# Optimization experiments

Hardware: AMD Instinct MI355X
Metric: run time of the kernel (lower is better)

## Reference

```python
import jax, jax.numpy as jnp
import numpy as np

N_HEAD = 16


def setup_inputs() -> dict:
    key = jax.random.key(0)
    ks = jax.random.split(key, 5)
    B, T, C = 4, 2048, 1024
    s = 1.0 / np.sqrt(C)
    x = jax.random.normal(ks[0], (B, T, C), dtype=jnp.float32)
    wq = jax.random.normal(ks[1], (C, C), dtype=jnp.float32) * s
    wk = jax.random.normal(ks[2], (C, C), dtype=jnp.float32) * s
    wv = jax.random.normal(ks[3], (C, C), dtype=jnp.float32) * s
    wo = jax.random.normal(ks[4], (C, C), dtype=jnp.float32) * s
    return {"x": x, "wq": wq, "wk": wk, "wv": wv, "wo": wo}


def _attn(x, wq, wk, wv, wo):
    B, T, C = x.shape
    H = N_HEAD
    D = C // H
    scale = 1.0 / np.sqrt(D)
    # nn.Linear(x) = x @ W.T; weights stored as [out, in]
    q = (x @ wq.T).reshape(B, T, H, D).transpose(0, 2, 1, 3)  # [B,H,T,D]
    k = (x @ wk.T).reshape(B, T, H, D).transpose(0, 2, 1, 3)
    v = (x @ wv.T).reshape(B, T, H, D).transpose(0, 2, 1, 3)
    scores = jnp.einsum("bhtd,bhsd->bhts", q, k) * scale  # [B,H,T,T]
    mask = jnp.triu(jnp.full((T, T), -jnp.inf, dtype=scores.dtype), k=1)
    attn = jax.nn.softmax(scores + mask, axis=-1)
    out = jnp.einsum("bhts,bhsd->bhtd", attn, v)  # [B,H,T,D]
    out = out.transpose(0, 2, 1, 3).reshape(B, T, C)
    return out @ wo.T


def reference(x, wq, wk, wv, wo):
    return _attn(x, wq, wk, wv, wo)
```

## Files before the change

kernel.cpp:

```cpp
#include <hip/hip_runtime.h>

typedef __bf16 bf16x8 __attribute__((ext_vector_type(8)));
typedef float f32x4 __attribute__((ext_vector_type(4)));
typedef unsigned short ushortx8 __attribute__((ext_vector_type(8)));
typedef unsigned short ushortx4 __attribute__((ext_vector_type(4)));

#if __has_builtin(__builtin_amdgcn_exp2f)
#define EXP2F(x) __builtin_amdgcn_exp2f(x)
#else
#define EXP2F(x) exp2f(x)
#endif
#if __has_builtin(__builtin_amdgcn_rcpf)
#define RCPF(x) __builtin_amdgcn_rcpf(x)
#else
#define RCPF(x) (1.0f / (x))
#endif

__device__ __forceinline__ unsigned short f2bf(float f) {
    unsigned int u = __builtin_bit_cast(unsigned int, f);
    u += 0x7fffu + ((u >> 16) & 1u);
    return (unsigned short)(u >> 16);
}

__device__ __forceinline__ bf16x8 ld_frag(const unsigned short* p) {
    return __builtin_bit_cast(bf16x8, *(const ushortx8*)p);
}

__device__ __forceinline__ unsigned int pack_bf2(float lo, float hi) {
#if __has_builtin(__builtin_amdgcn_cvt_pk_bf16_f32)
    typedef __bf16 bf16x2 __attribute__((ext_vector_type(2)));
    bf16x2 v = __builtin_amdgcn_cvt_pk_bf16_f32(lo, hi);
    return __builtin_bit_cast(unsigned int, v);
#else
    unsigned int ulo = __builtin_bit_cast(unsigned int, lo) + 0x8000u;
    unsigned int uhi = __builtin_bit_cast(unsigned int, hi) + 0x8000u;
    return __builtin_amdgcn_perm(uhi, ulo, 0x07060302u);
#endif
}

__device__ __forceinline__ void async_cp16(const unsigned short* g, unsigned short* l) {
    __builtin_amdgcn_global_load_lds(
        (const __attribute__((address_space(1))) unsigned int*)g,
        (__attribute__((address_space(3))) unsigned int*)(unsigned long)(unsigned long long)(uintptr_t)
            reinterpret_cast<uintptr_t>(l),
        16, 0, 0);
}

__global__ void cvt_kernel(const float* __restrict__ src, unsigned short* __restrict__ dst, int n4) {
    int i = blockIdx.x * blockDim.x + threadIdx.x;
    if (i < n4) {
        float4 f = ((const float4*)src)[i];
        ushortx4 u = { f2bf(f.x), f2bf(f.y), f2bf(f.z), f2bf(f.w) };
        ((ushortx4*)dst)[i] = u;
    }
}

__global__ void cvt4_kernel(const float* __restrict__ s0, const float* __restrict__ s1,
                            const float* __restrict__ s2, const float* __restrict__ s3,
                            unsigned short* __restrict__ dst) {
    const float* src = (blockIdx.y == 0) ? s0 : (blockIdx.y == 1) ? s1 : (blockIdx.y == 2) ? s2 : s3;
    unsigned short* d = dst + (size_t)blockIdx.y * (1024 * 1024);
    int i = blockIdx.x * blockDim.x + threadIdx.x;
    float4 f = ((const float4*)src)[i];
    ushortx4 u = { f2bf(f.x), f2bf(f.y), f2bf(f.z), f2bf(f.w) };
    ((ushortx4*)d)[i] = u;
}

__global__ __launch_bounds__(256, 2) void qkv_gemm(
    const unsigned short* __restrict__ xb,
    const unsigned short* __restrict__ wqb,
    const unsigned short* __restrict__ wkb,
    const unsigned short* __restrict__ wvb,
    unsigned short* __restrict__ q_ws,
    unsigned short* __restrict__ k_ws,
    unsigned short* __restrict__ v_ws)
{
    __shared__ __align__(16) unsigned short A_lds[128 * 32];
    __shared__ __align__(16) unsigned short B_lds[128 * 32];

    const int tid = threadIdx.x;
    const int wv = tid >> 6;
    const int lane = tid & 63;
    const int quad = lane >> 4;
    const int l15 = lane & 15;
    const int wm = wv >> 1;
    const int wn = wv & 1;

    const int m0 = blockIdx.x * 128;
    const int mat = blockIdx.y >> 3;
    const int n0 = (blockIdx.y & 7) * 128;
    const unsigned short* wb = (mat == 0) ? wqb : (mat == 1 ? wkb : wvb);

    const int srow = lane >> 2;
    const int scol = ((((lane & 3) - ((lane >> 3) & 3)) & 3) * 8);
    const unsigned short* ag0 = xb + (size_t)(m0 + wv * 32 + srow) * 1024 + scol;
    const unsigned short* ag1 = ag0 + 16 * 1024;
    const unsigned short* bg0 = wb + (size_t)(n0 + wv * 32 + srow) * 1024 + scol;
    const unsigned short* bg1 = bg0 + 16 * 1024;
    unsigned short* la0 = A_lds + (wv * 32) * 32;
    unsigned short* la1 = A_lds + (wv * 32 + 16) * 32;
    unsigned short* lb0 = B_lds + (wv * 32) * 32;
    unsigned short* lb1 = B_lds + (wv * 32 + 16) * 32;

    const int fcol = ((quad + (l15 >> 1)) & 3) * 8;

    f32x4 acc[4][4] = {};

    for (int kt = 0; kt < 1024; kt += 32) {
        __syncthreads();
        async_cp16(ag0 + kt, la0);
        async_cp16(ag1 + kt, la1);
        async_cp16(bg0 + kt, lb0);
        async_cp16(bg1 + kt, lb1);
        __builtin_amdgcn_s_waitcnt(0x0F70);
        __syncthreads();

        bf16x8 af[4], bf[4];
#pragma unroll
        for (int i = 0; i < 4; ++i)
            af[i] = ld_frag(A_lds + (wm * 64 + i * 16 + l15) * 32 + fcol);
#pragma unroll
        for (int i = 0; i < 4; ++i)
            bf[i] = ld_frag(B_lds + (wn * 64 + i * 16 + l15) * 32 + fcol);
#pragma unroll
        for (int i = 0; i < 4; ++i)
#pragma unroll
            for (int j = 0; j < 4; ++j)
                acc[i][j] = __builtin_amdgcn_mfma_f32_16x16x32_bf16(af[i], bf[j], acc[i][j], 0, 0, 0);
    }

    const float qscale = 0.125f * 1.4426950408889634f;
    const int mbase = m0 + wm * 64;
    const int nbase = n0 + wn * 64;
#pragma unroll
    for (int i = 0; i < 4; ++i) {
        const int mrow = mbase + i * 16 + quad * 4;
        const int b = mrow >> 11;
        const int trow = mrow & 2047;
#pragma unroll
        for (int j = 0; j < 4; ++j) {
            const int nloc = nbase + j * 16 + l15;
            const int h = nloc >> 6, d = nloc & 63;
            if (mat == 2) {
                ushortx4 pk = { f2bf(acc[i][j][0]), f2bf(acc[i][j][1]),
                                f2bf(acc[i][j][2]), f2bf(acc[i][j][3]) };
                *(ushortx4*)&v_ws[(((size_t)(b * 16 + h)) * 64 + d) * 2048 + trow] = pk;
            } else {
                unsigned short* dst = (mat == 0) ? q_ws : k_ws;
                float sc = (mat == 0) ? qscale : 1.0f;
                size_t base = (((size_t)(b * 16 + h)) * 2048 + trow) * 64 + d;
                dst[base]       = f2bf(acc[i][j][0] * sc);
                dst[base + 64]  = f2bf(acc[i][j][1] * sc);
                dst[base + 128] = f2bf(acc[i][j][2] * sc);
                dst[base + 192] = f2bf(acc[i][j][3] * sc);
            }
        }
    }
}

__global__ __launch_bounds__(256, 2) void attn_kernel(
    const unsigned short* __restrict__ q_ws,
    const unsigned short* __restrict__ k_ws,
    const unsigned short* __restrict__ v_ws,
    unsigned short* __restrict__ o_ws)
{
    __shared__ __align__(16) unsigned short K_lds[128 * 64];
    __shared__ __align__(16) unsigned short Vt_lds[64 * 128];
    __shared__ __align__(16) unsigned short P_lds[128][138];

    const int tid = threadIdx.x;
    const int wvid = tid >> 6, lane = tid & 63, quad = lane >> 4, l15 = lane & 15;
    const int bh = blockIdx.x;
    const int b = bh >> 4, h = bh & 15;
    const int bt = 15 - (int)blockIdx.y;
    const int t0 = bt * 128;

    const unsigned short* qb = q_ws + (size_t)bh * 2048 * 64;
    const unsigned short* kb = k_ws + (size_t)bh * 2048 * 64;
    const unsigned short* vb = v_ws + (size_t)bh * 64 * 2048;

    ushortx8 ones_u = { 0x3F80, 0x3F80, 0x3F80, 0x3F80, 0x3F80, 0x3F80, 0x3F80, 0x3F80 };
    const bf16x8 ones = __builtin_bit_cast(bf16x8, ones_u);

    bf16x8 bq[2][2];
#pragma unroll
    for (int it = 0; it < 2; ++it)
#pragma unroll
        for (int kk = 0; kk < 2; ++kk)
            bq[it][kk] = ld_frag(qb + (size_t)(t0 + wvid * 32 + it * 16 + l15) * 64 + kk * 32 + quad * 8);

    f32x4 acc_o[2][4] = {};
    f32x4 l_acc[2] = {};

    const int kr8 = lane >> 3, kp = lane & 7;
    const int vr4 = lane >> 4, vp = lane & 15;

    for (int j = 0; j <= bt; ++j) {
        const int s0 = j * 128;

        __syncthreads();
#pragma unroll
        for (int u = 0; u < 4; ++u) {
            const int rl = u * 32 + wvid * 8 + kr8;
            const int c = (kp - rl) & 7;
            async_cp16(kb + (size_t)(s0 + rl) * 64 + c * 8,
                       K_lds + (u * 32 + wvid * 8) * 64);
        }
#pragma unroll
        for (int u = 0; u < 4; ++u) {
            const int rl = u * 16 + wvid * 4 + vr4;
            const int c = (vp - rl) & 15;
            async_cp16(vb + (size_t)rl * 2048 + s0 + c * 8,
                       Vt_lds + (u * 16 + wvid * 4) * 128);
        }
        __builtin_amdgcn_s_waitcnt(0x0F70);
        __syncthreads();

        f32x4 sacc[2][8] = {};
#pragma unroll
        for (int is = 0; is < 8; ++is) {
            const int rK = is * 16 + l15;
            bf16x8 k0 = ld_frag(K_lds + rK * 64 + (((quad + rK) & 7) * 8));
            bf16x8 k1 = ld_frag(K_lds + rK * 64 + (((4 + quad + rK) & 7) * 8));
            sacc[0][is] = __builtin_amdgcn_mfma_f32_16x16x32_bf16(k0, bq[0][0], sacc[0][is], 0, 0, 0);
            sacc[0][is] = __builtin_amdgcn_mfma_f32_16x16x32_bf16(k1, bq[0][1], sacc[0][is], 0, 0, 0);
            sacc[1][is] = __builtin_amdgcn_mfma_f32_16x16x32_bf16(k0, bq[1][0], sacc[1][is], 0, 0, 0);
            sacc[1][is] = __builtin_amdgcn_mfma_f32_16x16x32_bf16(k1, bq[1][1], sacc[1][is], 0, 0, 0);
        }

        if (j == bt) {
#pragma unroll
            for (int it = 0; it < 2; ++it) {
                const int tl = wvid * 32 + it * 16 + l15;
#pragma unroll
                for (int is = 0; is < 8; ++is)
#pragma unroll
                    for (int r = 0; r < 4; ++r) {
                        const int sl = is * 16 + quad * 4 + r;
                        if (sl > tl) sacc[it][is][r] = -1.0e30f;
                    }
            }
        }

#pragma unroll
        for (int it = 0; it < 2; ++it) {
            const int row = wvid * 32 + it * 16 + l15;
#pragma unroll
            for (int is = 0; is < 8; ++is) {
                float p0 = EXP2F(sacc[it][is][0]);
                float p1 = EXP2F(sacc[it][is][1]);
                float p2 = EXP2F(sacc[it][is][2]);
                float p3 = EXP2F(sacc[it][is][3]);
                uint2 pk = { pack_bf2(p0, p1), pack_bf2(p2, p3) };
                *(uint2*)&P_lds[row][is * 16 + quad * 4] = pk;
            }
        }

        __threadfence_block();

#pragma unroll
        for (int kk = 0; kk < 4; ++kk) {
            bf16x8 p0 = ld_frag(&P_lds[wvid * 32 + l15][kk * 32 + quad * 8]);
            bf16x8 p1 = ld_frag(&P_lds[wvid * 32 + 16 + l15][kk * 32 + quad * 8]);
            l_acc[0] = __builtin_amdgcn_mfma_f32_16x16x32_bf16(p0, ones, l_acc[0], 0, 0, 0);
            l_acc[1] = __builtin_amdgcn_mfma_f32_16x16x32_bf16(p1, ones, l_acc[1], 0, 0, 0);
#pragma unroll
            for (int id = 0; id < 4; ++id) {
                const int rV = id * 16 + l15;
                bf16x8 bv = ld_frag(Vt_lds + rV * 128 + (((kk * 4 + quad + rV) & 15) * 8));
                acc_o[0][id] = __builtin_amdgcn_mfma_f32_16x16x32_bf16(p0, bv, acc_o[0][id], 0, 0, 0);
                acc_o[1][id] = __builtin_amdgcn_mfma_f32_16x16x32_bf16(p1, bv, acc_o[1][id], 0, 0, 0);
            }
        }
    }

#pragma unroll
    for (int it = 0; it < 2; ++it) {
        f32x4 rinv;
#pragma unroll
        for (int r = 0; r < 4; ++r) rinv[r] = RCPF(l_acc[it][r]);
#pragma unroll
        for (int id = 0; id < 4; ++id)
#pragma unroll
            for (int r = 0; r < 4; ++r) {
                int tg = t0 + wvid * 32 + it * 16 + quad * 4 + r;
                int c = h * 64 + id * 16 + l15;
                o_ws[(size_t)(b * 2048 + tg) * 1024 + c] = f2bf(acc_o[it][id][r] * rinv[r]);
            }
    }
}

__global__ __launch_bounds__(256, 2) void out_gemm(
    const unsigned short* __restrict__ ob,
    const unsigned short* __restrict__ wob,
    float* __restrict__ out)
{
    __shared__ __align__(16) unsigned short A_lds[128 * 32];
    __shared__ __align__(16) unsigned short B_lds[128 * 32];

    const int tid = threadIdx.x;
    const int wv = tid >> 6;
    const int lane = tid & 63;
    const int quad = lane >> 4;
    const int l15 = lane & 15;
    const int wm = wv >> 1;
    const int wn = wv & 1;

    const int m0 = blockIdx.x * 128;
    const int n0 = blockIdx.y * 128;

    const int srow = lane >> 2;
    const int scol = ((((lane & 3) - ((lane >> 3) & 3)) & 3) * 8);
    const unsigned short* ag0 = ob + (size_t)(m0 + wv * 32 + srow) * 1024 + scol;
    const unsigned short* ag1 = ag0 + 16 * 1024;
    const unsigned short* bg0 = wob + (size_t)(n0 + wv * 32 + srow) * 1024 + scol;
    const unsigned short* bg1 = bg0 + 16 * 1024;
    unsigned short* la0 = A_lds + (wv * 32) * 32;
    unsigned short* la1 = A_lds + (wv * 32 + 16) * 32;
    unsigned short* lb0 = B_lds + (wv * 32) * 32;
    unsigned short* lb1 = B_lds + (wv * 32 + 16) * 32;

    const int fcol = ((quad + (l15 >> 1)) & 3) * 8;

    f32x4 acc[4][4] = {};

    for (int kt = 0; kt < 1024; kt += 32) {
        __syncthreads();
        async_cp16(ag0 + kt, la0);
        async_cp16(ag1 + kt, la1);
        async_cp16(bg0 + kt, lb0);
        async_cp16(bg1 + kt, lb1);
        __builtin_amdgcn_s_waitcnt(0x0F70);
        __syncthreads();

        bf16x8 af[4], bf[4];
#pragma unroll
        for (int i = 0; i < 4; ++i)
            af[i] = ld_frag(A_lds + (wm * 64 + i * 16 + l15) * 32 + fcol);
#pragma unroll
        for (int i = 0; i < 4; ++i)
            bf[i] = ld_frag(B_lds + (wn * 64 + i * 16 + l15) * 32 + fcol);
#pragma unroll
        for (int i = 0; i < 4; ++i)
#pragma unroll
            for (int j = 0; j < 4; ++j)
                acc[i][j] = __builtin_amdgcn_mfma_f32_16x16x32_bf16(af[i], bf[j], acc[i][j], 0, 0, 0);
    }

    const int mbase = m0 + wm * 64;
    const int nbase = n0 + wn * 64;
#pragma unroll
    for (int i = 0; i < 4; ++i) {
        const int mrow = mbase + i * 16 + quad * 4;
#pragma unroll
        for (int j = 0; j < 4; ++j) {
            const int ncol = nbase + j * 16 + l15;
            float* dst = out + (size_t)mrow * 1024 + ncol;
            dst[0]        = acc[i][j][0];
            dst[1024]     = acc[i][j][1];
            dst[2048]     = acc[i][j][2];
            dst[3072]     = acc[i][j][3];
        }
    }
}

extern "C" void kernel_launch(void* const* d_in, const int* in_sizes, int n_in,
                              void* d_out, int out_size, void* d_ws, size_t ws_size,
                              hipStream_t stream) {
    const float* x  = (const float*)d_in[0];
    const float* wq = (const float*)d_in[1];
    const float* wk = (const float*)d_in[2];
    const float* wv = (const float*)d_in[3];
    const float* wo = (const float*)d_in[4];
    float* out = (float*)d_out;

    unsigned short* ws = (unsigned short*)d_ws;
    unsigned short* xb   = ws;
    unsigned short* wqb  = xb  + (size_t)8192 * 1024;
    unsigned short* wkb  = wqb + (size_t)1024 * 1024;
    unsigned short* wvb  = wkb + (size_t)1024 * 1024;
    unsigned short* wob  = wvb + (size_t)1024 * 1024;
    unsigned short* q_ws = wob + (size_t)1024 * 1024;
    unsigned short* k_ws = q_ws + (size_t)8192 * 1024;
    unsigned short* v_ws = k_ws + (size_t)8192 * 1024;
    unsigned short* o_ws = v_ws + (size_t)8192 * 1024;

    int n4 = (8192 * 1024) / 4;
    cvt_kernel<<<(n4 + 255) / 256, 256, 0, stream>>>(x, xb, n4);
    cvt4_kernel<<<dim3(1024, 4), 256, 0, stream>>>(wq, wk, wv, wo, wqb);

    qkv_gemm<<<dim3(64, 24), 256, 0, stream>>>(xb, wqb, wkb, wvb, q_ws, k_ws, v_ws);
    attn_kernel<<<dim3(64, 16), 256, 0, stream>>>(q_ws, k_ws, v_ws, o_ws);
    out_gemm<<<dim3(64, 8), 256, 0, stream>>>(o_ws, wob, out);
}
```

Baseline: 260.3 us.

## Double-buffer GEMM LDS tiles, register-prefetch K/V, skip masked diagonal work

Both projection GEMMs now use two LDS buffers so the next K-slice's async copy is in flight while MFMAs run on the current slice, and their launch bounds go from 2 to 3 blocks per CU. The attention kernel prefetches the next K/V tile into registers during compute and stores it to LDS at the top of the next iteration, instead of issuing a blocking async copy. On the diagonal tile it skips QK^T, exp and PV sub-blocks that are fully masked for each wave. The costs are double the GEMM shared memory, extra register pressure from the prefetch buffers and the tighter launch bound, and possible spills.

```diff
diff --git a/kernel.cpp b/kernel.cpp
--- a/kernel.cpp
+++ b/kernel.cpp
@@ -66,7 +66,7 @@
     ((ushortx4*)d)[i] = u;
 }
 
-__global__ __launch_bounds__(256, 2) void qkv_gemm(
+__global__ __launch_bounds__(256, 3) void qkv_gemm(
     const unsigned short* __restrict__ xb,
     const unsigned short* __restrict__ wqb,
     const unsigned short* __restrict__ wkb,
@@ -75,8 +75,8 @@
     unsigned short* __restrict__ k_ws,
     unsigned short* __restrict__ v_ws)
 {
-    __shared__ __align__(16) unsigned short A_lds[128 * 32];
-    __shared__ __align__(16) unsigned short B_lds[128 * 32];
+    __shared__ __align__(16) unsigned short A_lds[2][128 * 32];
+    __shared__ __align__(16) unsigned short B_lds[2][128 * 32];
 
     const int tid = threadIdx.x;
     const int wv = tid >> 6;
@@ -97,36 +97,45 @@
     const unsigned short* ag1 = ag0 + 16 * 1024;
     const unsigned short* bg0 = wb + (size_t)(n0 + wv * 32 + srow) * 1024 + scol;
     const unsigned short* bg1 = bg0 + 16 * 1024;
-    unsigned short* la0 = A_lds + (wv * 32) * 32;
-    unsigned short* la1 = A_lds + (wv * 32 + 16) * 32;
-    unsigned short* lb0 = B_lds + (wv * 32) * 32;
-    unsigned short* lb1 = B_lds + (wv * 32 + 16) * 32;
+    const int lo0 = (wv * 32) * 32;
+    const int lo1 = (wv * 32 + 16) * 32;
 
     const int fcol = ((quad + (l15 >> 1)) & 3) * 8;
 
     f32x4 acc[4][4] = {};
 
-    for (int kt = 0; kt < 1024; kt += 32) {
-        __syncthreads();
-        async_cp16(ag0 + kt, la0);
-        async_cp16(ag1 + kt, la1);
-        async_cp16(bg0 + kt, lb0);
-        async_cp16(bg1 + kt, lb1);
+    async_cp16(ag0, A_lds[0] + lo0);
+    async_cp16(ag1, A_lds[0] + lo1);
+    async_cp16(bg0, B_lds[0] + lo0);
+    async_cp16(bg1, B_lds[0] + lo1);
+    __builtin_amdgcn_s_waitcnt(0x0F70);
+    __syncthreads();
+
+    for (int i = 0; i < 32; ++i) {
+        const int cur = i & 1, nxt = cur ^ 1;
+        if (i < 31) {
+            const int kt = (i + 1) * 32;
+            async_cp16(ag0 + kt, A_lds[nxt] + lo0);
+            async_cp16(ag1 + kt, A_lds[nxt] + lo1);
+            async_cp16(bg0 + kt, B_lds[nxt] + lo0);
+            async_cp16(bg1 + kt, B_lds[nxt] + lo1);
+        }
+
+        bf16x8 af[4], bf[4];
+#pragma unroll
+        for (int ii = 0; ii < 4; ++ii)
+            af[ii] = ld_frag(A_lds[cur] + (wm * 64 + ii * 16 + l15) * 32 + fcol);
+#pragma unroll
+        for (int ii = 0; ii < 4; ++ii)
+            bf[ii] = ld_frag(B_lds[cur] + (wn * 64 + ii * 16 + l15) * 32 + fcol);
+#pragma unroll
+        for (int ii = 0; ii < 4; ++ii)
+#pragma unroll
+            for (int jj = 0; jj < 4; ++jj)
+                acc[ii][jj] = __builtin_amdgcn_mfma_f32_16x16x32_bf16(af[ii], bf[jj], acc[ii][jj], 0, 0, 0);
+
         __builtin_amdgcn_s_waitcnt(0x0F70);
         __syncthreads();
-
-        bf16x8 af[4], bf[4];
-#pragma unroll
-        for (int i = 0; i < 4; ++i)
-            af[i] = ld_frag(A_lds + (wm * 64 + i * 16 + l15) * 32 + fcol);
-#pragma unroll
-        for (int i = 0; i < 4; ++i)
-            bf[i] = ld_frag(B_lds + (wn * 64 + i * 16 + l15) * 32 + fcol);
-#pragma unroll
-        for (int i = 0; i < 4; ++i)
-#pragma unroll
-            for (int j = 0; j < 4; ++j)
-                acc[i][j] = __builtin_amdgcn_mfma_f32_16x16x32_bf16(af[i], bf[j], acc[i][j], 0, 0, 0);
     }
 
     const float qscale = 0.125f * 1.4426950408889634f;
@@ -192,8 +201,20 @@
     f32x4 acc_o[2][4] = {};
     f32x4 l_acc[2] = {};
 
-    const int kr8 = lane >> 3, kp = lane & 7;
-    const int vr4 = lane >> 4, vp = lane & 15;
+    const int krl = lane >> 3, kp = lane & 7;
+    const int vrl = lane >> 4, vp = lane & 15;
+
+    ushortx8 kreg[4], vreg[4];
+#pragma unroll
+    for (int u = 0; u < 4; ++u) {
+        const int rl = u * 32 + wvid * 8 + krl;
+        kreg[u] = *(const ushortx8*)(kb + (size_t)rl * 64 + (((kp - rl) & 7) * 8));
+    }
+#pragma unroll
+    for (int u = 0; u < 4; ++u) {
+        const int rl = u * 16 + wvid * 4 + vrl;
+        vreg[u] = *(const ushortx8*)(vb + (size_t)rl * 2048 + (((vp - rl) & 15) * 8));
+    }
 
     for (int j = 0; j <= bt; ++j) {
         const int s0 = j * 128;
@@ -201,32 +222,45 @@
         __syncthreads();
 #pragma unroll
         for (int u = 0; u < 4; ++u) {
-            const int rl = u * 32 + wvid * 8 + kr8;
-            const int c = (kp - rl) & 7;
-            async_cp16(kb + (size_t)(s0 + rl) * 64 + c * 8,
-                       K_lds + (u * 32 + wvid * 8) * 64);
+            const int rl = u * 32 + wvid * 8 + krl;
+            *(ushortx8*)&K_lds[rl * 64 + kp * 8] = kreg[u];
         }
 #pragma unroll
         for (int u = 0; u < 4; ++u) {
-            const int rl = u * 16 + wvid * 4 + vr4;
-            const int c = (vp - rl) & 15;
-            async_cp16(vb + (size_t)rl * 2048 + s0 + c * 8,
-                       Vt_lds + (u * 16 + wvid * 4) * 128);
-        }
-        __builtin_amdgcn_s_waitcnt(0x0F70);
+            const int rl = u * 16 + wvid * 4 + vrl;
+            *(ushortx8*)&Vt_lds[rl * 128 + vp * 8] = vreg[u];
+        }
         __syncthreads();
 
+        if (j < bt) {
+            const int s1 = s0 + 128;
+#pragma unroll
+            for (int u = 0; u < 4; ++u) {
+                const int rl = u * 32 + wvid * 8 + krl;
+                kreg[u] = *(const ushortx8*)(kb + (size_t)(s1 + rl) * 64 + (((kp - rl) & 7) * 8));
+            }
+#pragma unroll
+            for (int u = 0; u < 4; ++u) {
+                const int rl = u * 16 + wvid * 4 + vrl;
+                vreg[u] = *(const ushortx8*)(vb + (size_t)rl * 2048 + s1 + (((vp - rl) & 15) * 8));
+            }
+        }
+
+        const int is_lim = (j == bt) ? (wvid * 2 + 2) : 8;
+        const int kk_lim = (j == bt) ? (wvid + 1) : 4;
+
         f32x4 sacc[2][8] = {};
 #pragma unroll
-        for (int is = 0; is < 8; ++is) {
-            const int rK = is * 16 + l15;
-            bf16x8 k0 = ld_frag(K_lds + rK * 64 + (((quad + rK) & 7) * 8));
-            bf16x8 k1 = ld_frag(K_lds + rK * 64 + (((4 + quad + rK) & 7) * 8));
-            sacc[0][is] = __builtin_amdgcn_mfma_f32_16x16x32_bf16(k0, bq[0][0], sacc[0][is], 0, 0, 0);
-            sacc[0][is] = __builtin_amdgcn_mfma_f32_16x16x32_bf16(k1, bq[0][1], sacc[0][is], 0, 0, 0);
-            sacc[1][is] = __builtin_amdgcn_mfma_f32_16x16x32_bf16(k0, bq[1][0], sacc[1][is], 0, 0, 0);
-            sacc[1][is] = __builtin_amdgcn_mfma_f32_16x16x32_bf16(k1, bq[1][1], sacc[1][is], 0, 0, 0);
-        }
+        for (int is = 0; is < 8; ++is)
+            if (is < is_lim) {
+                const int rK = is * 16 + l15;
+                bf16x8 k0 = ld_frag(K_lds + rK * 64 + (((quad + rK) & 7) * 8));
+                bf16x8 k1 = ld_frag(K_lds + rK * 64 + (((4 + quad + rK) & 7) * 8));
+                sacc[0][is] = __builtin_amdgcn_mfma_f32_16x16x32_bf16(k0, bq[0][0], sacc[0][is], 0, 0, 0);
+                sacc[0][is] = __builtin_amdgcn_mfma_f32_16x16x32_bf16(k1, bq[0][1], sacc[0][is], 0, 0, 0);
+                sacc[1][is] = __builtin_amdgcn_mfma_f32_16x16x32_bf16(k0, bq[1][0], sacc[1][is], 0, 0, 0);
+                sacc[1][is] = __builtin_amdgcn_mfma_f32_16x16x32_bf16(k1, bq[1][1], sacc[1][is], 0, 0, 0);
+            }
 
         if (j == bt) {
 #pragma unroll
@@ -234,11 +268,12 @@
                 const int tl = wvid * 32 + it * 16 + l15;
 #pragma unroll
                 for (int is = 0; is < 8; ++is)
-#pragma unroll
-                    for (int r = 0; r < 4; ++r) {
-                        const int sl = is * 16 + quad * 4 + r;
-                        if (sl > tl) sacc[it][is][r] = -1.0e30f;
-                    }
+                    if (is < is_lim)
+#pragma unroll
+                        for (int r = 0; r < 4; ++r) {
+                            const int sl = is * 16 + quad * 4 + r;
+                            if (sl > tl) sacc[it][is][r] = -1.0e30f;
+                        }
             }
         }
 
@@ -246,32 +281,34 @@
         for (int it = 0; it < 2; ++it) {
             const int row = wvid * 32 + it * 16 + l15;
 #pragma unroll
-            for (int is = 0; is < 8; ++is) {
-                float p0 = EXP2F(sacc[it][is][0]);
-                float p1 = EXP2F(sacc[it][is][1]);
-                float p2 = EXP2F(sacc[it][is][2]);
-                float p3 = EXP2F(sacc[it][is][3]);
-                uint2 pk = { pack_bf2(p0, p1), pack_bf2(p2, p3) };
-                *(uint2*)&P_lds[row][is * 16 + quad * 4] = pk;
-            }
+            for (int is = 0; is < 8; ++is)
+                if (is < is_lim) {
+                    float p0 = EXP2F(sacc[it][is][0]);
+                    float p1 = EXP2F(sacc[it][is][1]);
+                    float p2 = EXP2F(sacc[it][is][2]);
+                    float p3 = EXP2F(sacc[it][is][3]);
+                    uint2 pk = { pack_bf2(p0, p1), pack_bf2(p2, p3) };
+                    *(uint2*)&P_lds[row][is * 16 + quad * 4] = pk;
+                }
         }
 
         __threadfence_block();
 
 #pragma unroll
-        for (int kk = 0; kk < 4; ++kk) {
-            bf16x8 p0 = ld_frag(&P_lds[wvid * 32 + l15][kk * 32 + quad * 8]);
-            bf16x8 p1 = ld_frag(&P_lds[wvid * 32 + 16 + l15][kk * 32 + quad * 8]);
-            l_acc[0] = __builtin_amdgcn_mfma_f32_16x16x32_bf16(p0, ones, l_acc[0], 0, 0, 0);
-            l_acc[1] = __builtin_amdgcn_mfma_f32_16x16x32_bf16(p1, ones, l_acc[1], 0, 0, 0);
-#pragma unroll
-            for (int id = 0; id < 4; ++id) {
-                const int rV = id * 16 + l15;
-                bf16x8 bv = ld_frag(Vt_lds + rV * 128 + (((kk * 4 + quad + rV) & 15) * 8));
-                acc_o[0][id] = __builtin_amdgcn_mfma_f32_16x16x32_bf16(p0, bv, acc_o[0][id], 0, 0, 0);
-                acc_o[1][id] = __builtin_amdgcn_mfma_f32_16x16x32_bf16(p1, bv, acc_o[1][id], 0, 0, 0);
-            }
-        }
+        for (int kk = 0; kk < 4; ++kk)
+            if (kk < kk_lim) {
+                bf16x8 p0 = ld_frag(&P_lds[wvid * 32 + l15][kk * 32 + quad * 8]);
+                bf16x8 p1 = ld_frag(&P_lds[wvid * 32 + 16 + l15][kk * 32 + quad * 8]);
+                l_acc[0] = __builtin_amdgcn_mfma_f32_16x16x32_bf16(p0, ones, l_acc[0], 0, 0, 0);
+                l_acc[1] = __builtin_amdgcn_mfma_f32_16x16x32_bf16(p1, ones, l_acc[1], 0, 0, 0);
+#pragma unroll
+                for (int id = 0; id < 4; ++id) {
+                    const int rV = id * 16 + l15;
+                    bf16x8 bv = ld_frag(Vt_lds + rV * 128 + (((kk * 4 + quad + rV) & 15) * 8));
+                    acc_o[0][id] = __builtin_amdgcn_mfma_f32_16x16x32_bf16(p0, bv, acc_o[0][id], 0, 0, 0);
+                    acc_o[1][id] = __builtin_amdgcn_mfma_f32_16x16x32_bf16(p1, bv, acc_o[1][id], 0, 0, 0);
+                }
+            }
     }
 
 #pragma unroll
@@ -290,13 +327,13 @@
     }
 }
 
-__global__ __launch_bounds__(256, 2) void out_gemm(
+__global__ __launch_bounds__(256, 3) void out_gemm(
     const unsigned short* __restrict__ ob,
     const unsigned short* __restrict__ wob,
     float* __restrict__ out)
 {
-    __shared__ __align__(16) unsigned short A_lds[128 * 32];
-    __shared__ __align__(16) unsigned short B_lds[128 * 32];
+    __shared__ __align__(16) unsigned short A_lds[2][128 * 32];
+    __shared__ __align__(16) unsigned short B_lds[2][128 * 32];
 
     const int tid = threadIdx.x;
     const int wv = tid >> 6;
@@ -315,36 +352,45 @@
     const unsigned short* ag1 = ag0 + 16 * 1024;
     const unsigned short* bg0 = wob + (size_t)(n0 + wv * 32 + srow) * 1024 + scol;
     const unsigned short* bg1 = bg0 + 16 * 1024;
-    unsigned short* la0 = A_lds + (wv * 32) * 32;
-    unsigned short* la1 = A_lds + (wv * 32 + 16) * 32;
-    unsigned short* lb0 = B_lds + (wv * 32) * 32;
-    unsigned short* lb1 = B_lds + (wv * 32 + 16) * 32;
+    const int lo0 = (wv * 32) * 32;
+    const int lo1 = (wv * 32 + 16) * 32;
 
     const int fcol = ((quad + (l15 >> 1)) & 3) * 8;
 
     f32x4 acc[4][4] = {};
 
-    for (int kt = 0; kt < 1024; kt += 32) {
-        __syncthreads();
-        async_cp16(ag0 + kt, la0);
-        async_cp16(ag1 + kt, la1);
-        async_cp16(bg0 + kt, lb0);
-        async_cp16(bg1 + kt, lb1);
+    async_cp16(ag0, A_lds[0] + lo0);
+    async_cp16(ag1, A_lds[0] + lo1);
+    async_cp16(bg0, B_lds[0] + lo0);
+    async_cp16(bg1, B_lds[0] + lo1);
+    __builtin_amdgcn_s_waitcnt(0x0F70);
+    __syncthreads();
+
+    for (int i = 0; i < 32; ++i) {
+        const int cur = i & 1, nxt = cur ^ 1;
+        if (i < 31) {
+            const int kt = (i + 1) * 32;
+            async_cp16(ag0 + kt, A_lds[nxt] + lo0);
+            async_cp16(ag1 + kt, A_lds[nxt] + lo1);
+            async_cp16(bg0 + kt, B_lds[nxt] + lo0);
+            async_cp16(bg1 + kt, B_lds[nxt] + lo1);
+        }
+
+        bf16x8 af[4], bf[4];
+#pragma unroll
+        for (int ii = 0; ii < 4; ++ii)
+            af[ii] = ld_frag(A_lds[cur] + (wm * 64 + ii * 16 + l15) * 32 + fcol);
+#pragma unroll
+        for (int ii = 0; ii < 4; ++ii)
+            bf[ii] = ld_frag(B_lds[cur] + (wn * 64 + ii * 16 + l15) * 32 + fcol);
+#pragma unroll
+        for (int ii = 0; ii < 4; ++ii)
+#pragma unroll
+            for (int jj = 0; jj < 4; ++jj)
+                acc[ii][jj] = __builtin_amdgcn_mfma_f32_16x16x32_bf16(af[ii], bf[jj], acc[ii][jj], 0, 0, 0);
+
         __builtin_amdgcn_s_waitcnt(0x0F70);
         __syncthreads();
-
-        bf16x8 af[4], bf[4];
-#pragma unroll
-        for (int i = 0; i < 4; ++i)
-            af[i] = ld_frag(A_lds + (wm * 64 + i * 16 + l15) * 32 + fcol);
-#pragma unroll
-        for (int i = 0; i < 4; ++i)
-            bf[i] = ld_frag(B_lds + (wn * 64 + i * 16 + l15) * 32 + fcol);
-#pragma unroll
-        for (int i = 0; i < 4; ++i)
-#pragma unroll
-            for (int j = 0; j < 4; ++j)
-                acc[i][j] = __builtin_amdgcn_mfma_f32_16x16x32_bf16(af[i], bf[j], acc[i][j], 0, 0, 0);
     }
 
     const int mbase = m0 + wm * 64;
```

Result: no change. 261.9 us (+0.6%).
